# Kernel optimization log

Measured on AMD Instinct MI355X. Metric: run time of the kernel, lower is better.

## Reference

```python
import jax, jax.numpy as jnp
import numpy as np

B, T, I, D = 16, 128, 8, 128


def layer_norm(x, g, b, eps=1e-5):
    mu = jnp.mean(x, -1, keepdims=True)
    var = jnp.mean((x - mu) ** 2, -1, keepdims=True)
    return (x - mu) * jax.lax.rsqrt(var + eps) * g + b


def setup_inputs() -> dict:
    key = jax.random.key(0)
    ks = jax.random.split(key, 8)
    vectors = jax.random.normal(ks[0], (B, T, T, I), jnp.float32)
    # structured pairwise mask: mask[b,i,j] = real[b,i] & real[b,j]
    lengths = jax.random.randint(ks[1], (B,), T // 2, T + 1)
    real = jnp.arange(T)[None, :] < lengths[:, None]  # [B,T]
    mask = real[:, :, None] & real[:, None, :]  # [B,T,T]
    s = lambda n: 1.0 / np.sqrt(n)
    W_embed = jax.random.normal(ks[2], (I, D), jnp.float32) * s(I)
    b_embed = jnp.zeros((D,), jnp.float32)
    ln1_g = jnp.ones((D,), jnp.float32)
    ln1_b = jnp.zeros((D,), jnp.float32)
    Wq = jax.random.normal(ks[3], (D, D), jnp.float32) * s(D)
    Wk = jax.random.normal(ks[4], (D, D), jnp.float32) * s(D)
    Wv = jax.random.normal(ks[5], (D, D), jnp.float32) * s(D)
    W_out = jax.random.normal(ks[6], (D, D), jnp.float32) * s(D)
    b_out = jnp.zeros((D,), jnp.float32)
    ln2_g = jnp.ones((D,), jnp.float32)
    ln2_b = jnp.zeros((D,), jnp.float32)
    return dict(vectors=vectors, mask=mask, W_embed=W_embed, b_embed=b_embed,
                ln1_g=ln1_g, ln1_b=ln1_b, Wq=Wq, Wk=Wk, Wv=Wv,
                W_out=W_out, b_out=b_out, ln2_g=ln2_g, ln2_b=ln2_b)


def reference(vectors, mask, W_embed, b_embed, ln1_g, ln1_b, Wq, Wk, Wv,
              W_out, b_out, ln2_g, ln2_b):
    Bs, Tn = vectors.shape[0], vectors.shape[1]
    Dm = W_embed.shape[1]
    square_mask = jnp.transpose(mask, (1, 2, 0))            # [T,T,B] bool
    seq = square_mask[jnp.arange(Tn), jnp.arange(Tn)]       # [T,B] bool (diagonal)
    # shared embedding stack (masked) + norm, on flattened [T*T,B,*]
    x = jnp.transpose(vectors.reshape(Bs, Tn * Tn, -1), (1, 0, 2))  # [T*T,B,I]
    mflat = square_mask.reshape(Tn * Tn, Bs, 1).astype(x.dtype)
    x = jax.nn.gelu(x @ W_embed + b_embed) * mflat
    x = layer_norm(x, ln1_g, ln1_b)
    x = x.reshape(Tn, Tn, Bs, Dm)                           # [T,T,B,D]
    keys = x @ Wk                                            # [T,T,B,D]
    values = x @ Wv                                          # [T,T,B,D]
    queries = x[jnp.arange(Tn), jnp.arange(Tn)] @ Wq         # diag gather -> [T,B,D]
    # attention mask: pairwise-real OR self
    amask = square_mask | jnp.eye(Tn, dtype=bool)[:, :, None]  # [T,T,B]
    logits = jnp.einsum('rbd,rcbd->rcb', queries, keys) / np.sqrt(Dm)
    logits = logits + jnp.where(amask, 0.0, -1e9)
    w = jax.nn.softmax(logits, axis=1)                       # [T,T,B]
    emb = jnp.einsum('rcb,rcbd->rbd', w, values)             # [T,B,D]
    # output linear block with skip connection, masked by sequence mask
    seq_f = seq[:, :, None].astype(emb.dtype)                # [T,B,1]
    h = jax.nn.gelu(emb @ W_out + b_out)
    embeddings = layer_norm(h + emb, ln2_g, ln2_b) * seq_f   # [T,B,D]
    padding_mask = ~jnp.transpose(seq)                       # [B,T]
    sequence_mask = seq[:, :, None]                          # [T,B,1]
    global_mask = jnp.ones((Tn,), dtype=bool)                # [T]
    return embeddings, padding_mask, sequence_mask, global_mask
```

## Files before the change

### kernel.cpp

```cpp
#include <hip/hip_runtime.h>
#include <hip/hip_fp16.h>
#include <math.h>

#define BB 16
#define TT 128
#define II 8
#define DD 128
#define SCALE 0.08838834764831845f

#define WS_WVO_OFF 16384
#define WS_LEN_OFF 32768


__device__ __forceinline__ float sgelu(float x) {
    float x2 = x * x;
    float w = x * (-1.5957691216f - 0.07135481627f * x2);
    float e = __expf(w);
    return __fdividef(x, 1.0f + e);
}

__device__ __forceinline__ float fast_gelu(float x) {
    float u = 1.5957691216057308f * x * (1.0f + 0.044715f * x * x);
    float e = __expf(u);
    float th = 1.0f - __fdividef(2.0f, e + 1.0f);
    return 0.5f * x * (1.0f + th);
}

__global__ void k0_setup(const float* __restrict__ Wq,
                         const float* __restrict__ Wk,
                         const float* __restrict__ Wv,
                         const float* __restrict__ Wo,
                         const int* __restrict__ mask,
                         float* __restrict__ M,
                         float* __restrict__ WvWo,
                         int* __restrict__ lens) {
    int blk = blockIdx.x;
    if (blk == DD) {
        __shared__ int cnt[BB];
        int t = threadIdx.x;
        if (t < BB) cnt[t] = 0;
        __syncthreads();
        for (int b = 0; b < BB; b++) {
            if (mask[b * TT * TT + t * TT + t]) atomicAdd(&cnt[b], 1);
        }
        __syncthreads();
        if (t < BB) lens[t] = cnt[t];
        return;
    }
    __shared__ float row[DD];
    int d = threadIdx.x;
    if (blk < DD) {
        int a = blk;
        row[d] = Wq[a * DD + d];
        __syncthreads();
        const float4* wk4 = (const float4*)(Wk + d * DD);
        float acc = 0.0f;
        #pragma unroll 8
        for (int e4 = 0; e4 < DD / 4; e4++) {
            float4 w = wk4[e4];
            acc += row[e4 * 4 + 0] * w.x + row[e4 * 4 + 1] * w.y +
                   row[e4 * 4 + 2] * w.z + row[e4 * 4 + 3] * w.w;
        }
        M[a * DD + d] = acc;
    } else {
        int a = blk - DD - 1;
        row[d] = Wv[a * DD + d];
        __syncthreads();
        float acc = 0.0f;
        #pragma unroll 8
        for (int e = 0; e < DD; e++) acc += row[e] * Wo[e * DD + d];
        WvWo[a * DD + d] = acc;
    }
}

__global__ __launch_bounds__(256, 4)
void k_main(const float* __restrict__ vectors,
            const int* __restrict__ lens,
            const float* __restrict__ We,
            const float* __restrict__ be,
            const float* __restrict__ g1,
            const float* __restrict__ b1,
            const float* __restrict__ M,
            const float* __restrict__ Wv,
            const float* __restrict__ WvWo,
            const float* __restrict__ bo,
            const float* __restrict__ g2,
            const float* __restrict__ b2,
            float* __restrict__ out) {
    __shared__ __half2 xsh[TT * 64];
    __shared__ float  xrs[DD];
    __shared__ float2 kq2s[64];
    __shared__ float2 us2[64];
    __shared__ float  mus[TT];
    __shared__ float  rstds[TT];
    __shared__ float  lgt[TT];
    __shared__ float  wgt4[4 * TT];
    __shared__ float2 pbuf[256];
    __shared__ float2 sv2[64];

    int n = blockIdx.x;
    int b = n >> 7, r = n & 127;
    int t = threadIdx.x, wave = t >> 6, lane = t & 63;
    int hh = lane >> 5, sl = lane & 31;
    int dl = sl * 4;
    int len = lens[b];

    if (r >= len) {
        if (wave == 0) {
            int rb_out = r * BB + b;
            ((float2*)out)[rb_out * 64 + lane] = make_float2(0.0f, 0.0f);
            if (lane == 0) {
                out[262144 + b * TT + r] = 1.0f;
                out[264192 + r * BB + b] = 0.0f;
                if (b == 0) out[266240 + r] = 1.0f;
            }
        }
        return;
    }

    const float4* vb4 = (const float4*)(vectors + (size_t)n * TT * II);

    float4 we4[II];
    #pragma unroll
    for (int i = 0; i < II; i++) we4[i] = *(const float4*)(We + i * DD + dl);
    float4 be4 = *(const float4*)(be + dl);
    float4 g14 = *(const float4*)(g1 + dl);
    float4 b14 = *(const float4*)(b1 + dl);

    {
        int g = (wave << 1) + hh;
        int jmax = (len - g + 15) >> 4;
        for (int j = 0; j < jmax; j++) {
            int cA = (j << 4) + g;
            int cB = cA + 8;
            float4 vA0 = vb4[2 * cA], vA1 = vb4[2 * cA + 1];
            float4 vB0 = vb4[2 * cB], vB1 = vb4[2 * cB + 1];
            float vA[8] = {vA0.x, vA0.y, vA0.z, vA0.w, vA1.x, vA1.y, vA1.z, vA1.w};
            float vB[8] = {vB0.x, vB0.y, vB0.z, vB0.w, vB1.x, vB1.y, vB1.z, vB1.w};
            float eA0 = be4.x, eA1 = be4.y, eA2 = be4.z, eA3 = be4.w;
            float eB0 = be4.x, eB1 = be4.y, eB2 = be4.z, eB3 = be4.w;
            #pragma unroll
            for (int i = 0; i < II; i++) {
                eA0 += vA[i] * we4[i].x; eA1 += vA[i] * we4[i].y;
                eA2 += vA[i] * we4[i].z; eA3 += vA[i] * we4[i].w;
                eB0 += vB[i] * we4[i].x; eB1 += vB[i] * we4[i].y;
                eB2 += vB[i] * we4[i].z; eB3 += vB[i] * we4[i].w;
            }
            float aA0 = sgelu(eA0), aA1 = sgelu(eA1), aA2 = sgelu(eA2), aA3 = sgelu(eA3);
            float aB0 = sgelu(eB0), aB1 = sgelu(eB1), aB2 = sgelu(eB2), aB3 = sgelu(eB3);
            float sA = (aA0 + aA1) + (aA2 + aA3);
            float qA = (aA0 * aA0 + aA1 * aA1) + (aA2 * aA2 + aA3 * aA3);
            float sB = (aB0 + aB1) + (aB2 + aB3);
            float qB = (aB0 * aB0 + aB1 * aB1) + (aB2 * aB2 + aB3 * aB3);
            #pragma unroll
            for (int o = 16; o >= 1; o >>= 1) {
                sA += __shfl_xor(sA, o, 64); qA += __shfl_xor(qA, o, 64);
                sB += __shfl_xor(sB, o, 64); qB += __shfl_xor(qB, o, 64);
            }
            float muA = sA * (1.0f / 128.0f), muB = sB * (1.0f / 128.0f);
            float rsA = rsqrtf(qA * (1.0f / 128.0f) - muA * muA + 1e-5f);
            float rsB = rsqrtf(qB * (1.0f / 128.0f) - muB * muB + 1e-5f);
            {
                __half2 p0 = __floats2half2_rn(aA0, aA1), p1 = __floats2half2_rn(aA2, aA3);
                uint2 st; st.x = *(unsigned*)&p0; st.y = *(unsigned*)&p1;
                ((uint2*)(xsh + cA * 64))[sl] = st;
                if (sl == 0) { mus[cA] = muA; rstds[cA] = rsA; }
                if (cA == r) {
                    ((float4*)xrs)[sl] = make_float4(
                        (aA0 - muA) * rsA * g14.x + b14.x,
                        (aA1 - muA) * rsA * g14.y + b14.y,
                        (aA2 - muA) * rsA * g14.z + b14.z,
                        (aA3 - muA) * rsA * g14.w + b14.w);
                }
            }
            if (cB < len) {
                __half2 p0 = __floats2half2_rn(aB0, aB1), p1 = __floats2half2_rn(aB2, aB3);
                uint2 st; st.x = *(unsigned*)&p0; st.y = *(unsigned*)&p1;
                ((uint2*)(xsh + cB * 64))[sl] = st;
                if (sl == 0) { mus[cB] = muB; rstds[cB] = rsB; }
                if (cB == r) {
                    ((float4*)xrs)[sl] = make_float4(
                        (aB0 - muB) * rsB * g14.x + b14.x,
                        (aB1 - muB) * rsB * g14.y + b14.y,
                        (aB2 - muB) * rsB * g14.z + b14.z,
                        (aB3 - muB) * rsB * g14.w + b14.w);
                }
            }
        }
    }
    __syncthreads();

    {
        const float2* M2 = (const float2*)M;
        float ax = 0.0f, ay = 0.0f;
        #pragma unroll 8
        for (int j = 0; j < 32; j++) {
            int a = (wave << 5) + j;
            float xv = xrs[a];
            float2 m2 = M2[a * 64 + lane];
            ax += xv * m2.x; ay += xv * m2.y;
        }
        pbuf[t] = make_float2(ax, ay);
    }
    __syncthreads();
    if (t < 64) {
        float2 p0 = pbuf[t], p1 = pbuf[64 + t], p2 = pbuf[128 + t], p3 = pbuf[192 + t];
        float k0 = (p0.x + p1.x + p2.x + p3.x) * SCALE;
        float k1 = (p0.y + p1.y + p2.y + p3.y) * SCALE;
        kq2s[t] = make_float2(k0, k1);
        float2 g1v = ((const float2*)g1)[t];
        us2[t] = make_float2(k0 * g1v.x, k1 * g1v.y);
    }
    __syncthreads();

    float Us, C0;
    {
        float2 uu = us2[lane];
        float2 kk = kq2s[lane];
        float2 bb = ((const float2*)b1)[lane];
        float usp = uu.x + uu.y;
        float c0p = bb.x * kk.x + bb.y * kk.y;
        #pragma unroll
        for (int o = 32; o >= 1; o >>= 1) {
            usp += __shfl_xor(usp, o, 64); c0p += __shfl_xor(c0p, o, 64);
        }
        Us = usp; C0 = c0p;
    }

    {
        int c = t >> 1, p = t & 1;
        if (c < len) {
            float acc = 0.0f;
            #pragma unroll 8
            for (int j = 0; j < 32; j++) {
                int idx = (p << 5) + ((j + c) & 31);
                float2 xf = __half22float2(xsh[c * 64 + idx]);
                float2 uv = us2[idx];
                acc += xf.x * uv.x + xf.y * uv.y;
            }
            acc += __shfl_xor(acc, 1, 64);
            if (p == 0) lgt[c] = rstds[c] * (acc - mus[c] * Us) + C0;
        }
    }
    __syncthreads();

    float invS, Aterm;
    {
        float l0 = lgt[lane];
        bool v1 = (lane + 64 < len);
        float l1 = v1 ? lgt[lane + 64] : -1e9f;
        float mx = fmaxf(l0, l1);
        #pragma unroll
        for (int o = 32; o >= 1; o >>= 1) mx = fmaxf(mx, __shfl_xor(mx, o, 64));
        float e0 = __expf(l0 - mx), e1 = __expf(l1 - mx);
        float er0 = e0 * rstds[lane];
        float er1 = v1 ? e1 * rstds[lane + 64] : 0.0f;
        float sp = e0 + e1;
        float ap = er0 * mus[lane] + (v1 ? er1 * mus[lane + 64] : 0.0f);
        #pragma unroll
        for (int o = 32; o >= 1; o >>= 1) {
            sp += __shfl_xor(sp, o, 64); ap += __shfl_xor(ap, o, 64);
        }
        invS = __fdividef(1.0f, sp);
        Aterm = ap;
        wgt4[(wave << 7) + lane] = er0;
        wgt4[(wave << 7) + lane + 64] = er1;
    }

    {
        int wb = wave << 7;
        int jw = (len - wave + 3) >> 2;
        float ax = 0.0f, ay = 0.0f;
        for (int j = 0; j < jw; j++) {
            int c = (j << 2) + wave;
            float v = wgt4[wb + c];
            float2 xf = __half22float2(xsh[c * 64 + lane]);
            ax += v * xf.x; ay += v * xf.y;
        }
        pbuf[t] = make_float2(ax, ay);
    }
    __syncthreads();
    if (t < 64) {
        float2 p0 = pbuf[t], p1 = pbuf[64 + t], p2 = pbuf[128 + t], p3 = pbuf[192 + t];
        float Ux = p0.x + p1.x + p2.x + p3.x;
        float Uy = p0.y + p1.y + p2.y + p3.y;
        float2 g1v = ((const float2*)g1)[t];
        float2 b1v = ((const float2*)b1)[t];
        sv2[t] = make_float2(g1v.x * (Ux - Aterm) * invS + b1v.x,
                             g1v.y * (Uy - Aterm) * invS + b1v.y);
    }
    __syncthreads();

    {
        const float* svf = (const float*)sv2;
        const float2* W2 = (wave < 2) ? (const float2*)Wv : (const float2*)WvWo;
        int abase = (wave & 1) << 6;
        float ax = 0.0f, ay = 0.0f;
        #pragma unroll 8
        for (int j = 0; j < 64; j++) {
            int a = abase + j;
            float s = svf[a];
            float2 w2 = W2[a * 64 + lane];
            ax += s * w2.x; ay += s * w2.y;
        }
        pbuf[t] = make_float2(ax, ay);
    }
    __syncthreads();

    if (wave == 0) {
        float2 e0 = pbuf[lane], e1 = pbuf[64 + lane];
        float2 h0p = pbuf[128 + lane], h1p = pbuf[192 + lane];
        float2 bo2 = ((const float2*)bo)[lane];
        float em0 = e0.x + e1.x, em1 = e0.y + e1.y;
        float h0 = fast_gelu(h0p.x + h1p.x + bo2.x);
        float h1 = fast_gelu(h0p.y + h1p.y + bo2.y);
        float z0 = h0 + em0, z1 = h1 + em1;
        float s = z0 + z1, q = z0 * z0 + z1 * z1;
        #pragma unroll
        for (int o = 32; o >= 1; o >>= 1) {
            s += __shfl_xor(s, o, 64); q += __shfl_xor(q, o, 64);
        }
        float mu = s * (1.0f / 128.0f);
        float rstd = rsqrtf(q * (1.0f / 128.0f) - mu * mu + 1e-5f);
        float2 g22 = ((const float2*)g2)[lane], b22 = ((const float2*)b2)[lane];
        float u0 = z0 - mu, u1 = z1 - mu;
        int rb_out = r * BB + b;
        ((float2*)out)[rb_out * 64 + lane] =
            make_float2(u0 * rstd * g22.x + b22.x,
                        u1 * rstd * g22.y + b22.y);
        if (lane == 0) {
            out[262144 + b * TT + r] = 0.0f;
            out[264192 + r * BB + b] = 1.0f;
            if (b == 0) out[266240 + r] = 1.0f;
        }
    }
}

extern "C" void kernel_launch(void* const* d_in, const int* in_sizes, int n_in,
                              void* d_out, int out_size, void* d_ws, size_t ws_size,
                              hipStream_t stream) {
    const float* vectors = (const float*)d_in[0];
    const int*   mask    = (const int*)d_in[1];
    const float* W_embed = (const float*)d_in[2];
    const float* b_embed = (const float*)d_in[3];
    const float* ln1_g   = (const float*)d_in[4];
    const float* ln1_b   = (const float*)d_in[5];
    const float* Wq      = (const float*)d_in[6];
    const float* Wk      = (const float*)d_in[7];
    const float* Wv      = (const float*)d_in[8];
    const float* W_out   = (const float*)d_in[9];
    const float* b_out   = (const float*)d_in[10];
    const float* ln2_g   = (const float*)d_in[11];
    const float* ln2_b   = (const float*)d_in[12];
    float* out = (float*)d_out;

    float* M    = (float*)d_ws;
    float* WvWo = (float*)d_ws + WS_WVO_OFF;
    int*   lens = (int*)((float*)d_ws + WS_LEN_OFF);

    hipLaunchKernelGGL(k0_setup, dim3(2 * DD + 1), dim3(DD), 0, stream,
                       Wq, Wk, Wv, W_out, mask, M, WvWo, lens);
    hipLaunchKernelGGL(k_main, dim3(TT * BB), dim3(256), 0, stream,
                       vectors, lens, W_embed, b_embed, ln1_g, ln1_b, M,
                       Wv, WvWo, b_out, ln2_g, ln2_b, out);
}
```

Measured before the change: 137.7 us.

## Double block size to 512 threads and reduce partials via shared atomics

The main kernel now runs 512 threads per block, so each wave handles half as many rows and columns in the embedding, logits, weighted-sum and projection stages. Cross-wave partial sums now go through shared-memory atomicAdd into zeroed accumulators instead of a pbuf buffer followed by a serial reduction. The aim is more parallelism per row block to hide latency. The cost is atomic contention, extra zero-initialisation, and higher register and LDS pressure from the changed launch bounds.

```diff
diff --git a/kernel.cpp b/kernel.cpp
--- a/kernel.cpp
+++ b/kernel.cpp
@@ -73,7 +73,7 @@
     }
 }
 
-__global__ __launch_bounds__(256, 4)
+__global__ __launch_bounds__(512, 6)
 void k_main(const float* __restrict__ vectors,
             const int* __restrict__ lens,
             const float* __restrict__ We,
@@ -89,14 +89,15 @@
             float* __restrict__ out) {
     __shared__ __half2 xsh[TT * 64];
     __shared__ float  xrs[DD];
-    __shared__ float2 kq2s[64];
+    __shared__ float  kqacc[DD];
     __shared__ float2 us2[64];
     __shared__ float  mus[TT];
     __shared__ float  rstds[TT];
     __shared__ float  lgt[TT];
-    __shared__ float  wgt4[4 * TT];
-    __shared__ float2 pbuf[256];
-    __shared__ float2 sv2[64];
+    __shared__ float  wgt[TT];
+    __shared__ float  svacc[DD];
+    __shared__ float  embacc[DD];
+    __shared__ float  hacc[DD];
 
     int n = blockIdx.x;
     int b = n >> 7, r = n & 127;
@@ -118,6 +119,8 @@
         return;
     }
 
+    if (t < DD) { kqacc[t] = 0.0f; svacc[t] = 0.0f; embacc[t] = 0.0f; hacc[t] = 0.0f; }
+
     const float4* vb4 = (const float4*)(vectors + (size_t)n * TT * II);
 
     float4 we4[II];
@@ -129,10 +132,10 @@
 
     {
         int g = (wave << 1) + hh;
-        int jmax = (len - g + 15) >> 4;
+        int jmax = (len - g + 31) >> 5;
         for (int j = 0; j < jmax; j++) {
-            int cA = (j << 4) + g;
-            int cB = cA + 8;
+            int cA = (j << 5) + g;
+            int cB = cA + 16;
             float4 vA0 = vb4[2 * cA], vA1 = vb4[2 * cA + 1];
             float4 vB0 = vb4[2 * cB], vB1 = vb4[2 * cB + 1];
             float vA[8] = {vA0.x, vA0.y, vA0.z, vA0.w, vA1.x, vA1.y, vA1.z, vA1.w};
@@ -192,34 +195,34 @@
 
     {
         const float2* M2 = (const float2*)M;
+        int a0 = wave << 4;
         float ax = 0.0f, ay = 0.0f;
-        #pragma unroll 8
-        for (int j = 0; j < 32; j++) {
-            int a = (wave << 5) + j;
+        #pragma unroll
+        for (int j = 0; j < 16; j++) {
+            int a = a0 + j;
             float xv = xrs[a];
             float2 m2 = M2[a * 64 + lane];
             ax += xv * m2.x; ay += xv * m2.y;
         }
-        pbuf[t] = make_float2(ax, ay);
-    }
-    __syncthreads();
+        atomicAdd(&kqacc[2 * lane], ax);
+        atomicAdd(&kqacc[2 * lane + 1], ay);
+    }
+    __syncthreads();
+
     if (t < 64) {
-        float2 p0 = pbuf[t], p1 = pbuf[64 + t], p2 = pbuf[128 + t], p3 = pbuf[192 + t];
-        float k0 = (p0.x + p1.x + p2.x + p3.x) * SCALE;
-        float k1 = (p0.y + p1.y + p2.y + p3.y) * SCALE;
-        kq2s[t] = make_float2(k0, k1);
+        float k0v = kqacc[2 * t] * SCALE, k1v = kqacc[2 * t + 1] * SCALE;
         float2 g1v = ((const float2*)g1)[t];
-        us2[t] = make_float2(k0 * g1v.x, k1 * g1v.y);
+        us2[t] = make_float2(k0v * g1v.x, k1v * g1v.y);
     }
     __syncthreads();
 
     float Us, C0;
     {
         float2 uu = us2[lane];
-        float2 kk = kq2s[lane];
         float2 bb = ((const float2*)b1)[lane];
+        float kx = kqacc[2 * lane] * SCALE, ky = kqacc[2 * lane + 1] * SCALE;
         float usp = uu.x + uu.y;
-        float c0p = bb.x * kk.x + bb.y * kk.y;
+        float c0p = bb.x * kx + bb.y * ky;
         #pragma unroll
         for (int o = 32; o >= 1; o >>= 1) {
             usp += __shfl_xor(usp, o, 64); c0p += __shfl_xor(c0p, o, 64);
@@ -228,17 +231,18 @@
     }
 
     {
-        int c = t >> 1, p = t & 1;
+        int c = t >> 2, p = t & 3;
         if (c < len) {
             float acc = 0.0f;
-            #pragma unroll 8
-            for (int j = 0; j < 32; j++) {
-                int idx = (p << 5) + ((j + c) & 31);
+            #pragma unroll
+            for (int j = 0; j < 16; j++) {
+                int idx = (p << 4) + ((j + c) & 15);
                 float2 xf = __half22float2(xsh[c * 64 + idx]);
                 float2 uv = us2[idx];
                 acc += xf.x * uv.x + xf.y * uv.y;
             }
             acc += __shfl_xor(acc, 1, 64);
+            acc += __shfl_xor(acc, 2, 64);
             if (p == 0) lgt[c] = rstds[c] * (acc - mus[c] * Us) + C0;
         }
     }
@@ -252,7 +256,8 @@
         float mx = fmaxf(l0, l1);
         #pragma unroll
         for (int o = 32; o >= 1; o >>= 1) mx = fmaxf(mx, __shfl_xor(mx, o, 64));
-        float e0 = __expf(l0 - mx), e1 = __expf(l1 - mx);
+        float e0 = __expf(l0 - mx);
+        float e1 = v1 ? __expf(l1 - mx) : 0.0f;
         float er0 = e0 * rstds[lane];
         float er1 = v1 ? e1 * rstds[lane + 64] : 0.0f;
         float sp = e0 + e1;
@@ -263,57 +268,55 @@
         }
         invS = __fdividef(1.0f, sp);
         Aterm = ap;
-        wgt4[(wave << 7) + lane] = er0;
-        wgt4[(wave << 7) + lane + 64] = er1;
-    }
-
-    {
-        int wb = wave << 7;
-        int jw = (len - wave + 3) >> 2;
+        wgt[lane] = er0;
+        wgt[lane + 64] = er1;
+    }
+
+    {
+        int jw = (len - wave + 7) >> 3;
         float ax = 0.0f, ay = 0.0f;
         for (int j = 0; j < jw; j++) {
-            int c = (j << 2) + wave;
-            float v = wgt4[wb + c];
+            int c = (j << 3) + wave;
+            float v = wgt[c];
             float2 xf = __half22float2(xsh[c * 64 + lane]);
             ax += v * xf.x; ay += v * xf.y;
         }
-        pbuf[t] = make_float2(ax, ay);
-    }
-    __syncthreads();
+        atomicAdd(&svacc[2 * lane], ax);
+        atomicAdd(&svacc[2 * lane + 1], ay);
+    }
+    __syncthreads();
+
     if (t < 64) {
-        float2 p0 = pbuf[t], p1 = pbuf[64 + t], p2 = pbuf[128 + t], p3 = pbuf[192 + t];
-        float Ux = p0.x + p1.x + p2.x + p3.x;
-        float Uy = p0.y + p1.y + p2.y + p3.y;
+        float Ux = svacc[2 * t], Uy = svacc[2 * t + 1];
         float2 g1v = ((const float2*)g1)[t];
         float2 b1v = ((const float2*)b1)[t];
-        sv2[t] = make_float2(g1v.x * (Ux - Aterm) * invS + b1v.x,
-                             g1v.y * (Uy - Aterm) * invS + b1v.y);
-    }
-    __syncthreads();
-
-    {
-        const float* svf = (const float*)sv2;
-        const float2* W2 = (wave < 2) ? (const float2*)Wv : (const float2*)WvWo;
-        int abase = (wave & 1) << 6;
+        xrs[2 * t]     = g1v.x * (Ux - Aterm) * invS + b1v.x;
+        xrs[2 * t + 1] = g1v.y * (Uy - Aterm) * invS + b1v.y;
+    }
+    __syncthreads();
+
+    {
+        const float2* W2 = (wave < 4) ? (const float2*)Wv : (const float2*)WvWo;
+        float* accp = (wave < 4) ? embacc : hacc;
+        int a0 = (wave & 3) << 5;
         float ax = 0.0f, ay = 0.0f;
         #pragma unroll 8
-        for (int j = 0; j < 64; j++) {
-            int a = abase + j;
-            float s = svf[a];
+        for (int j = 0; j < 32; j++) {
+            int a = a0 + j;
+            float s = xrs[a];
             float2 w2 = W2[a * 64 + lane];
             ax += s * w2.x; ay += s * w2.y;
         }
-        pbuf[t] = make_float2(ax, ay);
+        atomicAdd(&accp[2 * lane], ax);
+        atomicAdd(&accp[2 * lane + 1], ay);
     }
     __syncthreads();
 
     if (wave == 0) {
-        float2 e0 = pbuf[lane], e1 = pbuf[64 + lane];
-        float2 h0p = pbuf[128 + lane], h1p = pbuf[192 + lane];
+        float em0 = embacc[2 * lane], em1 = embacc[2 * lane + 1];
         float2 bo2 = ((const float2*)bo)[lane];
-        float em0 = e0.x + e1.x, em1 = e0.y + e1.y;
-        float h0 = fast_gelu(h0p.x + h1p.x + bo2.x);
-        float h1 = fast_gelu(h0p.y + h1p.y + bo2.y);
+        float h0 = fast_gelu(hacc[2 * lane] + bo2.x);
+        float h1 = fast_gelu(hacc[2 * lane + 1] + bo2.y);
         float z0 = h0 + em0, z1 = h1 + em1;
         float s = z0 + z1, q = z0 * z0 + z1 * z1;
         #pragma unroll
@@ -360,7 +363,7 @@
 
     hipLaunchKernelGGL(k0_setup, dim3(2 * DD + 1), dim3(DD), 0, stream,
                        Wq, Wk, Wv, W_out, mask, M, WvWo, lens);
-    hipLaunchKernelGGL(k_main, dim3(TT * BB), dim3(256), 0, stream,
+    hipLaunchKernelGGL(k_main, dim3(TT * BB), dim3(512), 0, stream,
                        vectors, lens, W_embed, b_embed, ln1_g, ln1_b, M,
                        Wv, WvWo, b_out, ln2_g, ln2_b, out);
 }
```

Result: slower. 163.5 us (+18.8%).
